# Performance work log

Measured on AMD Instinct MI355X. Metric: run time of the kernel, lower is better.

Reference implementation:

```python
import jax, jax.numpy as jnp
import numpy as np

N_NODES = 100000


def gcn_conv(x, W, b, row, col, n_nodes):
    # PyG GCNConv: x' = D^{-1/2} (A + I) D^{-1/2} (x W) + b
    xw = x @ W  # [N, out]
    ones = jnp.ones(row.shape[0], dtype=x.dtype)
    deg = jnp.zeros((n_nodes,), dtype=x.dtype).at[col].add(ones) + 1.0  # +1 self-loop
    dinv = jax.lax.rsqrt(deg)
    norm = dinv[row] * dinv[col]  # per-edge normalization [E]
    msgs = xw[row] * norm[:, None]  # gather + scale [E, out]
    agg = jax.ops.segment_sum(msgs, col, num_segments=n_nodes)
    # self-loop contribution: norm = deg^{-1/2} * deg^{-1/2} = 1/deg
    agg = agg + xw * (1.0 / deg)[:, None]
    return agg + b


def setup_inputs() -> dict:
    key = jax.random.key(0)
    k1, k2, k3, k4 = jax.random.split(key, 4)
    x = jax.random.normal(k1, (N_NODES, 128), dtype=jnp.float32)
    edge_index = jax.random.randint(k2, (2, 1600000), 0, N_NODES, dtype=jnp.int64)
    W1 = jax.random.normal(k3, (128, 256), dtype=jnp.float32) * (1.0 / np.sqrt(128))
    b1 = jnp.zeros((256,), dtype=jnp.float32)
    W2 = jax.random.normal(k4, (256, 128), dtype=jnp.float32) * (1.0 / np.sqrt(256))
    b2 = jnp.zeros((128,), dtype=jnp.float32)
    return {"x": x, "edge_index": edge_index, "W1": W1, "b1": b1, "W2": W2, "b2": b2}


def reference(x, edge_index, W1, b1, W2, b2):
    row, col = edge_index[0], edge_index[1]
    n = x.shape[0]
    h = gcn_conv(x, W1, b1, row, col, n)
    h = jax.nn.gelu(h)
    out = gcn_conv(h, W2, b2, row, col, n)
    return out
```

## Files before the change

### kernel.cpp

```cpp
#include <hip/hip_runtime.h>
#include <hip/hip_bf16.h>
#include <math.h>

typedef __attribute__((ext_vector_type(8))) short bf16x8;
typedef __attribute__((ext_vector_type(4))) float f32x4;

__device__ inline ushort f2bf(float f) {
    uint u = __float_as_uint(f);
    uint r = u + 0x7fffu + ((u >> 16) & 1u);
    return (ushort)(r >> 16);
}
__device__ inline float bf2f(ushort h) { return __uint_as_float(((uint)h) << 16); }

__device__ inline float gelu_fast(float x) {
    float z2 = 1.5957691216057308f * (x + 0.044715f * x * x * x);
    return x / (1.0f + __expf(-z2));
}


__global__ void deg_rank_kernel(const int* __restrict__ col, int* __restrict__ deg64,
                                int* __restrict__ rank, int E) {
    int e = blockIdx.x * blockDim.x + threadIdx.x;
    if (e < E) rank[e] = atomicAdd(&deg64[col[e] << 4], 1);
}

__global__ void dinv_kernel(const int* __restrict__ deg64, float* __restrict__ dinv,
                            int* __restrict__ deg, int M) {
    int i = blockIdx.x * blockDim.x + threadIdx.x;
    if (i < M) {
        int d = deg64[i << 4];
        deg[i] = d;
        dinv[i] = rsqrtf((float)d + 1.0f);
    }
}


__global__ void block_reduce_kernel(const int* __restrict__ deg, int* __restrict__ bsum, int M) {
    __shared__ int s[256];
    int i = blockIdx.x * 256 + threadIdx.x;
    s[threadIdx.x] = (i < M) ? deg[i] : 0;
    __syncthreads();
    for (int o = 128; o > 0; o >>= 1) {
        if (threadIdx.x < o) s[threadIdx.x] += s[threadIdx.x + o];
        __syncthreads();
    }
    if (threadIdx.x == 0) bsum[blockIdx.x] = s[0];
}

__global__ void scan_bsum_kernel(int* __restrict__ bsum, int nb) {
    __shared__ int s[512];
    int t = threadIdx.x;
    int orig = (t < nb) ? bsum[t] : 0;
    s[t] = orig;
    __syncthreads();
    for (int o = 1; o < 512; o <<= 1) {
        int v = 0;
        if (t >= o) v = s[t - o];
        __syncthreads();
        if (t >= o) s[t] += v;
        __syncthreads();
    }
    if (t < nb) bsum[t] = s[t] - orig;
}

__global__ void scan_offsets_kernel(const int* __restrict__ deg, const int* __restrict__ bsum,
                                    int* __restrict__ off, int M) {
    __shared__ int s[256];
    int i = blockIdx.x * 256 + threadIdx.x;
    int orig = (i < M) ? deg[i] : 0;
    s[threadIdx.x] = orig;
    __syncthreads();
    for (int o = 1; o < 256; o <<= 1) {
        int v = 0;
        if (threadIdx.x >= o) v = s[threadIdx.x - o];
        __syncthreads();
        if (threadIdx.x >= o) s[threadIdx.x] += v;
        __syncthreads();
    }
    if (i < M) off[i] = bsum[blockIdx.x] + s[threadIdx.x] - orig;
}


__global__ void fill_sorted_kernel(const int* __restrict__ row, const int* __restrict__ col,
                                   const int* __restrict__ off, const int* __restrict__ rank,
                                   int* __restrict__ rs, int E) {
    int e = blockIdx.x * blockDim.x + threadIdx.x;
    if (e < E) rs[off[col[e]] + rank[e]] = row[e];
}


__global__ void prep_weights(const float* __restrict__ W1, const float* __restrict__ W2,
                             ushort* __restrict__ wt1, ushort* __restrict__ wt2) {
    int idx = blockIdx.x * 256 + threadIdx.x;
    if (idx < 128 * 256) {
        int k = idx >> 8, n = idx & 255;
        wt1[n * 128 + k] = f2bf(W1[idx]);
    } else if (idx < 2 * 128 * 256) {
        int i2 = idx - 128 * 256;
        int k = i2 >> 7, n = i2 & 127;
        wt2[n * 256 + k] = f2bf(W2[i2]);
    }
}


__global__ void to_bf16_scaled_kernel(const float* __restrict__ in, const float* __restrict__ dinv,
                                      ushort* __restrict__ out, int n8) {
    int i = blockIdx.x * 256 + threadIdx.x;
    if (i >= n8) return;
    float s = dinv[i >> 4];
    float4 a = *(const float4*)(in + (size_t)i * 8);
    float4 b = *(const float4*)(in + (size_t)i * 8 + 4);
    ushort4 u0 = make_ushort4(f2bf(a.x * s), f2bf(a.y * s), f2bf(a.z * s), f2bf(a.w * s));
    ushort4 u1 = make_ushort4(f2bf(b.x * s), f2bf(b.y * s), f2bf(b.z * s), f2bf(b.w * s));
    *(ushort4*)(out + (size_t)i * 8) = u0;
    *(ushort4*)(out + (size_t)i * 8 + 4) = u1;
}


__global__ __launch_bounds__(256, 2) void gemm_fused(const ushort* __restrict__ A,
                                                     const ushort* __restrict__ wt1,
                                                     const float* __restrict__ b1,
                                                     const ushort* __restrict__ wt2,
                                                     const float* __restrict__ dinv,
                                                     ushort* __restrict__ Cb, int M) {
    __shared__ ushort lh[64 * 256];

    const int t = threadIdx.x;
    const int R0 = blockIdx.x * 64;
    const int w = t >> 6, l = t & 63;
    const int lrow = l & 15;
    const int lk = l >> 4;

    bf16x8 w1[4][4];
    {
        const int c0 = w * 64;
        #pragma unroll
        for (int n = 0; n < 4; ++n) {
            int oc = c0 + n * 16 + lrow;
            #pragma unroll
            for (int ks = 0; ks < 4; ++ks) {
                int kb = ks * 32 + lk * 8;
                w1[n][ks] = *(const bf16x8*)&wt1[(size_t)oc * 128 + kb];
            }
        }
    }

    {
        const int c0 = w * 64;
        f32x4 acc[4][4] = {};
        #pragma unroll
        for (int ks = 0; ks < 4; ++ks) {
            const int kb = ks * 32 + lk * 8;
            bf16x8 xf[4];
            #pragma unroll
            for (int m = 0; m < 4; ++m) {
                int gr = R0 + m * 16 + lrow;
                gr = gr < M ? gr : M - 1;
                xf[m] = *(const bf16x8*)(A + (size_t)gr * 128 + kb);
            }
            #pragma unroll
            for (int n = 0; n < 4; ++n)
                #pragma unroll
                for (int m = 0; m < 4; ++m)
                    acc[n][m] = __builtin_amdgcn_mfma_f32_16x16x32_bf16(w1[n][ks], xf[m], acc[n][m], 0, 0, 0);
        }
        #pragma unroll
        for (int n = 0; n < 4; ++n) {
            int ob = c0 + n * 16 + lk * 4;
            float4 bb = *(const float4*)(b1 + ob);
            #pragma unroll
            for (int m = 0; m < 4; ++m) {
                int nd = m * 16 + lrow;
                ushort4 pk;
                pk.x = f2bf(gelu_fast(acc[n][m][0] + bb.x));
                pk.y = f2bf(gelu_fast(acc[n][m][1] + bb.y));
                pk.z = f2bf(gelu_fast(acc[n][m][2] + bb.z));
                pk.w = f2bf(gelu_fast(acc[n][m][3] + bb.w));
                int byte = (nd * 256 + ob) * 2;
                byte ^= (nd & 7) << 4;
                *(ushort4*)((char*)lh + byte) = pk;
            }
        }
    }

    bf16x8 w2[2][8];
    {
        const int c0 = w * 32;
        #pragma unroll
        for (int n = 0; n < 2; ++n) {
            int oc = c0 + n * 16 + lrow;
            #pragma unroll
            for (int ks = 0; ks < 8; ++ks) {
                int kb = ks * 32 + lk * 8;
                w2[n][ks] = *(const bf16x8*)&wt2[(size_t)oc * 256 + kb];
            }
        }
    }
    __syncthreads();

    {
        const int c0 = w * 32;
        f32x4 acc2[2][4] = {};
        #pragma unroll
        for (int ks = 0; ks < 8; ++ks) {
            const int kb = ks * 32 + lk * 8;
            bf16x8 hf[4];
            #pragma unroll
            for (int m = 0; m < 4; ++m) {
                int nd = m * 16 + lrow;
                int byte = (nd * 256 + kb) * 2;
                byte ^= (nd & 7) << 4;
                hf[m] = *(const bf16x8*)((const char*)lh + byte);
            }
            #pragma unroll
            for (int n = 0; n < 2; ++n)
                #pragma unroll
                for (int m = 0; m < 4; ++m)
                    acc2[n][m] = __builtin_amdgcn_mfma_f32_16x16x32_bf16(w2[n][ks], hf[m], acc2[n][m], 0, 0, 0);
        }
        #pragma unroll
        for (int m = 0; m < 4; ++m) {
            int nd = m * 16 + lrow;
            int grow = R0 + nd;
            if (grow < M) {
                float sc = dinv[grow];
                #pragma unroll
                for (int n = 0; n < 2; ++n) {
                    int ob = c0 + n * 16 + lk * 4;
                    ushort4 pk;
                    pk.x = f2bf(acc2[n][m][0] * sc);
                    pk.y = f2bf(acc2[n][m][1] * sc);
                    pk.z = f2bf(acc2[n][m][2] * sc);
                    pk.w = f2bf(acc2[n][m][3] * sc);
                    *(ushort4*)(Cb + (size_t)grow * 128 + ob) = pk;
                }
            }
        }
    }
}


template <bool BIAS, bool OUTBF>
__global__ __launch_bounds__(256) void gather_sum_kernel(const int* __restrict__ off,
                                                         const int* __restrict__ deg,
                                                         const int* __restrict__ rs,
                                                         const float* __restrict__ dinv,
                                                         const ushort* __restrict__ srcb,
                                                         const float* __restrict__ b,
                                                         float* __restrict__ dstf,
                                                         ushort* __restrict__ dstb, int M) {
    int wid = (blockIdx.x * 256 + threadIdx.x) >> 6;
    int lane = threadIdx.x & 63;
    int grp = lane >> 4;
    int l16 = lane & 15;
    if (wid >= M) return;
    int s0 = off[wid];
    int n = deg[wid];
    float acc[8] = {};
    float acc2[8] = {};

    if (grp == 0) {
        bf16x8 u = *(const bf16x8*)(srcb + (size_t)wid * 128 + l16 * 8);
        #pragma unroll
        for (int i = 0; i < 8; ++i) acc[i] += bf2f((ushort)u[i]);
    }

    int j = 0;
    for (; j + 8 <= n; j += 8) {
        int r0 = rs[s0 + j + grp];
        int r1 = rs[s0 + j + 4 + grp];
        bf16x8 u0 = *(const bf16x8*)(srcb + (size_t)r0 * 128 + l16 * 8);
        bf16x8 u1 = *(const bf16x8*)(srcb + (size_t)r1 * 128 + l16 * 8);
        #pragma unroll
        for (int i = 0; i < 8; ++i) {
            acc[i] += bf2f((ushort)u0[i]);
            acc2[i] += bf2f((ushort)u1[i]);
        }
    }
    if (j + 4 <= n) {
        int r = rs[s0 + j + grp];
        bf16x8 u = *(const bf16x8*)(srcb + (size_t)r * 128 + l16 * 8);
        #pragma unroll
        for (int i = 0; i < 8; ++i) acc[i] += bf2f((ushort)u[i]);
        j += 4;
    }
    if (j + grp < n) {
        int r = rs[s0 + j + grp];
        bf16x8 u = *(const bf16x8*)(srcb + (size_t)r * 128 + l16 * 8);
        #pragma unroll
        for (int i = 0; i < 8; ++i) acc2[i] += bf2f((ushort)u[i]);
    }

    #pragma unroll
    for (int i = 0; i < 8; ++i) {
        acc[i] += acc2[i];
        acc[i] += __shfl_xor(acc[i], 16);
        acc[i] += __shfl_xor(acc[i], 32);
    }

    if (grp == 0) {
        float sc = dinv[wid];
        #pragma unroll
        for (int i = 0; i < 8; ++i) acc[i] *= sc;
        if constexpr (BIAS) {
            float4 b0 = *(const float4*)(b + l16 * 8);
            float4 b1v = *(const float4*)(b + l16 * 8 + 4);
            acc[0] += b0.x; acc[1] += b0.y; acc[2] += b0.z; acc[3] += b0.w;
            acc[4] += b1v.x; acc[5] += b1v.y; acc[6] += b1v.z; acc[7] += b1v.w;
        }
        if constexpr (OUTBF) {
            bf16x8 o;
            #pragma unroll
            for (int i = 0; i < 8; ++i) o[i] = (short)f2bf(acc[i]);
            *(bf16x8*)(dstb + (size_t)wid * 128 + l16 * 8) = o;
        } else {
            float4 o0 = make_float4(acc[0], acc[1], acc[2], acc[3]);
            float4 o1 = make_float4(acc[4], acc[5], acc[6], acc[7]);
            *(float4*)(dstf + (size_t)wid * 128 + l16 * 8) = o0;
            *(float4*)(dstf + (size_t)wid * 128 + l16 * 8 + 4) = o1;
        }
    }
}


extern "C" void kernel_launch(void* const* d_in, const int* in_sizes, int n_in,
                              void* d_out, int out_size, void* d_ws, size_t ws_size,
                              hipStream_t stream) {
    const float* x  = (const float*)d_in[0];
    const int*   ei = (const int*)d_in[1];
    const float* W1 = (const float*)d_in[2];
    const float* b1 = (const float*)d_in[3];
    const float* W2 = (const float*)d_in[4];
    const float* b2 = (const float*)d_in[5];

    const int M = in_sizes[0] / 128;
    const int E = in_sizes[1] / 2;
    const int* row = ei;
    const int* col = ei + E;

    ushort* xb    = (ushort*)d_ws;
    ushort* aggxb = xb + 12800000;
    ushort* xw2b  = aggxb;
    float*  dinv  = (float*)(aggxb + 12800000);
    int*    deg64 = (int*)(dinv + 102400);
    int*    deg   = deg64 + 1638400;
    int*    off   = deg + 102400;
    int*    rank  = off + 102400;
    int*    rs    = rank + 1600000;
    int*    bsum  = rs + 1600000;
    ushort* wt1   = (ushort*)(bsum + 1024);
    ushort* wt2   = wt1 + 32768;
    float*  outw  = (float*)d_out;

    const int nb = (M + 255) / 256;

    hipMemsetAsync(deg64, 0, (size_t)1638400 * sizeof(int), stream);

    deg_rank_kernel<<<(E + 255) / 256, 256, 0, stream>>>(col, deg64, rank, E);
    dinv_kernel<<<(M + 255) / 256, 256, 0, stream>>>(deg64, dinv, deg, M);

    block_reduce_kernel<<<nb, 256, 0, stream>>>(deg, bsum, M);
    scan_bsum_kernel<<<1, 512, 0, stream>>>(bsum, nb);
    scan_offsets_kernel<<<nb, 256, 0, stream>>>(deg, bsum, off, M);

    fill_sorted_kernel<<<(E + 255) / 256, 256, 0, stream>>>(row, col, off, rank, rs, E);

    prep_weights<<<256, 256, 0, stream>>>(W1, W2, wt1, wt2);
    to_bf16_scaled_kernel<<<(M * 16 + 255) / 256, 256, 0, stream>>>(x, dinv, xb, M * 16);

    gather_sum_kernel<false, true><<<(M * 64 + 255) / 256, 256, 0, stream>>>(
        off, deg, rs, dinv, xb, nullptr, nullptr, aggxb, M);

    gemm_fused<<<(M + 63) / 64, 256, 0, stream>>>(aggxb, wt1, b1, wt2, dinv, xw2b, M);

    gather_sum_kernel<true, false><<<(M * 64 + 255) / 256, 256, 0, stream>>>(
        off, deg, rs, dinv, xw2b, b2, outw, nullptr, M);
}
```

Before: 301.8 us.

## Fuse prep kernels, pre-pack MFMA weight fragments, stage A tile in LDS

Merges the dinv computation with the block reduction, and merges the weight conversion with the x-to-bf16 scaling, removing two kernel launches. Weights are now written in the per-lane MFMA fragment order, so the GEMM loads them as contiguous coalesced 16-byte reads. The GEMM also stages its 64x128 input tile into swizzled LDS with coalesced loads instead of strided per-lane global reads. This adds 16 KB of LDS per block and an extra barrier, which may reduce occupancy.

```diff
diff --git a/kernel.cpp b/kernel.cpp
--- a/kernel.cpp
+++ b/kernel.cpp
@@ -24,21 +24,17 @@
     if (e < E) rank[e] = atomicAdd(&deg64[col[e] << 4], 1);
 }
 
-__global__ void dinv_kernel(const int* __restrict__ deg64, float* __restrict__ dinv,
-                            int* __restrict__ deg, int M) {
-    int i = blockIdx.x * blockDim.x + threadIdx.x;
+__global__ void dinv_reduce_kernel(const int* __restrict__ deg64, float* __restrict__ dinv,
+                                   int* __restrict__ deg, int* __restrict__ bsum, int M) {
+    __shared__ int s[256];
+    int i = blockIdx.x * 256 + threadIdx.x;
+    int d = 0;
     if (i < M) {
-        int d = deg64[i << 4];
+        d = deg64[i << 4];
         deg[i] = d;
         dinv[i] = rsqrtf((float)d + 1.0f);
     }
-}
-
-
-__global__ void block_reduce_kernel(const int* __restrict__ deg, int* __restrict__ bsum, int M) {
-    __shared__ int s[256];
-    int i = blockIdx.x * 256 + threadIdx.x;
-    s[threadIdx.x] = (i < M) ? deg[i] : 0;
+    s[threadIdx.x] = d;
     __syncthreads();
     for (int o = 128; o > 0; o >>= 1) {
         if (threadIdx.x < o) s[threadIdx.x] += s[threadIdx.x + o];
@@ -89,40 +85,52 @@
 }
 
 
-__global__ void prep_weights(const float* __restrict__ W1, const float* __restrict__ W2,
-                             ushort* __restrict__ wt1, ushort* __restrict__ wt2) {
-    int idx = blockIdx.x * 256 + threadIdx.x;
-    if (idx < 128 * 256) {
-        int k = idx >> 8, n = idx & 255;
-        wt1[n * 128 + k] = f2bf(W1[idx]);
-    } else if (idx < 2 * 128 * 256) {
-        int i2 = idx - 128 * 256;
-        int k = i2 >> 7, n = i2 & 127;
-        wt2[n * 256 + k] = f2bf(W2[i2]);
-    }
-}
-
-
-__global__ void to_bf16_scaled_kernel(const float* __restrict__ in, const float* __restrict__ dinv,
-                                      ushort* __restrict__ out, int n8) {
-    int i = blockIdx.x * 256 + threadIdx.x;
-    if (i >= n8) return;
-    float s = dinv[i >> 4];
-    float4 a = *(const float4*)(in + (size_t)i * 8);
-    float4 b = *(const float4*)(in + (size_t)i * 8 + 4);
-    ushort4 u0 = make_ushort4(f2bf(a.x * s), f2bf(a.y * s), f2bf(a.z * s), f2bf(a.w * s));
-    ushort4 u1 = make_ushort4(f2bf(b.x * s), f2bf(b.y * s), f2bf(b.z * s), f2bf(b.w * s));
-    *(ushort4*)(out + (size_t)i * 8) = u0;
-    *(ushort4*)(out + (size_t)i * 8 + 4) = u1;
+__global__ void prep_convert_kernel(const float* __restrict__ x, const float* __restrict__ dinv,
+                                    const float* __restrict__ W1, const float* __restrict__ W2,
+                                    ushort* __restrict__ xb, ushort* __restrict__ p1,
+                                    ushort* __restrict__ p2, int n8) {
+    int t = blockIdx.x * 256 + threadIdx.x;
+    if (t < n8) {
+        float s = dinv[t >> 4];
+        float4 a = *(const float4*)(x + (size_t)t * 8);
+        float4 b = *(const float4*)(x + (size_t)t * 8 + 4);
+        ushort4 u0 = make_ushort4(f2bf(a.x * s), f2bf(a.y * s), f2bf(a.z * s), f2bf(a.w * s));
+        ushort4 u1 = make_ushort4(f2bf(b.x * s), f2bf(b.y * s), f2bf(b.z * s), f2bf(b.w * s));
+        *(ushort4*)(xb + (size_t)t * 8) = u0;
+        *(ushort4*)(xb + (size_t)t * 8 + 4) = u1;
+        return;
+    }
+    int u = t - n8;
+    if (u < 4096) {
+        int g = u >> 6, l = u & 63;
+        int w = g >> 4, n = (g >> 2) & 3, ks = g & 3;
+        int oc = w * 64 + n * 16 + (l & 15);
+        int kb = ks * 32 + (l >> 4) * 8;
+        ushort tmp[8];
+        #pragma unroll
+        for (int j = 0; j < 8; ++j) tmp[j] = f2bf(W1[(size_t)(kb + j) * 256 + oc]);
+        *(bf16x8*)(p1 + (size_t)u * 8) = *(bf16x8*)tmp;
+    } else if (u < 8192) {
+        int v = u - 4096;
+        int g = v >> 6, l = v & 63;
+        int w = g >> 4, n = (g >> 3) & 1, ks = g & 7;
+        int oc = w * 32 + n * 16 + (l & 15);
+        int kb = ks * 32 + (l >> 4) * 8;
+        ushort tmp[8];
+        #pragma unroll
+        for (int j = 0; j < 8; ++j) tmp[j] = f2bf(W2[(size_t)(kb + j) * 128 + oc]);
+        *(bf16x8*)(p2 + (size_t)v * 8) = *(bf16x8*)tmp;
+    }
 }
 
 
 __global__ __launch_bounds__(256, 2) void gemm_fused(const ushort* __restrict__ A,
-                                                     const ushort* __restrict__ wt1,
+                                                     const ushort* __restrict__ p1,
                                                      const float* __restrict__ b1,
-                                                     const ushort* __restrict__ wt2,
+                                                     const ushort* __restrict__ p2,
                                                      const float* __restrict__ dinv,
                                                      ushort* __restrict__ Cb, int M) {
+    __shared__ ushort la[64 * 128];
     __shared__ ushort lh[64 * 256];
 
     const int t = threadIdx.x;
@@ -131,32 +139,37 @@
     const int lrow = l & 15;
     const int lk = l >> 4;
 
+    #pragma unroll
+    for (int base = 0; base < 1024; base += 256) {
+        int idx = base + t;
+        int r = idx >> 4;
+        int c8 = idx & 15;
+        int gr = R0 + r;
+        gr = gr < M ? gr : M - 1;
+        bf16x8 v = *(const bf16x8*)(A + (size_t)gr * 128 + c8 * 8);
+        int byte = idx * 16 ^ ((r & 7) << 4);
+        *(bf16x8*)((char*)la + byte) = v;
+    }
+
     bf16x8 w1[4][4];
-    {
-        const int c0 = w * 64;
-        #pragma unroll
-        for (int n = 0; n < 4; ++n) {
-            int oc = c0 + n * 16 + lrow;
-            #pragma unroll
-            for (int ks = 0; ks < 4; ++ks) {
-                int kb = ks * 32 + lk * 8;
-                w1[n][ks] = *(const bf16x8*)&wt1[(size_t)oc * 128 + kb];
-            }
-        }
-    }
+    #pragma unroll
+    for (int n = 0; n < 4; ++n)
+        #pragma unroll
+        for (int ks = 0; ks < 4; ++ks)
+            w1[n][ks] = *(const bf16x8*)(p1 + (size_t)(((w * 4 + n) * 4 + ks) * 64 + l) * 8);
+    __syncthreads();
 
     {
         const int c0 = w * 64;
         f32x4 acc[4][4] = {};
         #pragma unroll
         for (int ks = 0; ks < 4; ++ks) {
-            const int kb = ks * 32 + lk * 8;
             bf16x8 xf[4];
             #pragma unroll
             for (int m = 0; m < 4; ++m) {
-                int gr = R0 + m * 16 + lrow;
-                gr = gr < M ? gr : M - 1;
-                xf[m] = *(const bf16x8*)(A + (size_t)gr * 128 + kb);
+                int nd = m * 16 + lrow;
+                int byte = (nd * 256 + ks * 64 + lk * 16) ^ ((nd & 7) << 4);
+                xf[m] = *(const bf16x8*)((const char*)la + byte);
             }
             #pragma unroll
             for (int n = 0; n < 4; ++n)
@@ -184,18 +197,11 @@
     }
 
     bf16x8 w2[2][8];
-    {
-        const int c0 = w * 32;
-        #pragma unroll
-        for (int n = 0; n < 2; ++n) {
-            int oc = c0 + n * 16 + lrow;
-            #pragma unroll
-            for (int ks = 0; ks < 8; ++ks) {
-                int kb = ks * 32 + lk * 8;
-                w2[n][ks] = *(const bf16x8*)&wt2[(size_t)oc * 256 + kb];
-            }
-        }
-    }
+    #pragma unroll
+    for (int n = 0; n < 2; ++n)
+        #pragma unroll
+        for (int ks = 0; ks < 8; ++ks)
+            w2[n][ks] = *(const bf16x8*)(p2 + (size_t)(((w * 2 + n) * 8 + ks) * 64 + l) * 8);
     __syncthreads();
 
     {
@@ -348,8 +354,8 @@
     int*    rank  = off + 102400;
     int*    rs    = rank + 1600000;
     int*    bsum  = rs + 1600000;
-    ushort* wt1   = (ushort*)(bsum + 1024);
-    ushort* wt2   = wt1 + 32768;
+    ushort* p1    = (ushort*)(bsum + 1024);
+    ushort* p2    = p1 + 32768;
     float*  outw  = (float*)d_out;
 
     const int nb = (M + 255) / 256;
@@ -357,21 +363,18 @@
     hipMemsetAsync(deg64, 0, (size_t)1638400 * sizeof(int), stream);
 
     deg_rank_kernel<<<(E + 255) / 256, 256, 0, stream>>>(col, deg64, rank, E);
-    dinv_kernel<<<(M + 255) / 256, 256, 0, stream>>>(deg64, dinv, deg, M);
-
-    block_reduce_kernel<<<nb, 256, 0, stream>>>(deg, bsum, M);
+    dinv_reduce_kernel<<<nb, 256, 0, stream>>>(deg64, dinv, deg, bsum, M);
     scan_bsum_kernel<<<1, 512, 0, stream>>>(bsum, nb);
     scan_offsets_kernel<<<nb, 256, 0, stream>>>(deg, bsum, off, M);
-
     fill_sorted_kernel<<<(E + 255) / 256, 256, 0, stream>>>(row, col, off, rank, rs, E);
 
-    prep_weights<<<256, 256, 0, stream>>>(W1, W2, wt1, wt2);
-    to_bf16_scaled_kernel<<<(M * 16 + 255) / 256, 256, 0, stream>>>(x, dinv, xb, M * 16);
+    prep_convert_kernel<<<(M * 16 + 8192 + 255) / 256, 256, 0, stream>>>(
+        x, dinv, W1, W2, xb, p1, p2, M * 16);
 
     gather_sum_kernel<false, true><<<(M * 64 + 255) / 256, 256, 0, stream>>>(
         off, deg, rs, dinv, xb, nullptr, nullptr, aggxb, M);
 
-    gemm_fused<<<(M + 63) / 64, 256, 0, stream>>>(aggxb, wt1, b1, wt2, dinv, xw2b, M);
+    gemm_fused<<<(M + 63) / 64, 256, 0, stream>>>(aggxb, p1, b1, p2, dinv, xw2b, M);
 
     gather_sum_kernel<true, false><<<(M * 64 + 255) / 256, 256, 0, stream>>>(
         off, deg, rs, dinv, xw2b, b2, outw, nullptr, M);
```

New measurement: 278.2 us. 7.8% less time.
